# Kernel tuning notes

Hardware: AMD Instinct MI355X
Metric: run time of the kernel (lower is better)

The kernel has to match this reference:

```python
import jax, jax.numpy as jnp
import numpy as np

ALPHA = 30.0  # init kwarg alpha
K = 16        # init kwarg k


def setup_inputs() -> dict:
    key = jax.random.key(0)
    k1, k2 = jax.random.split(key)
    x = jax.random.normal(k1, (4096, 1024), dtype=jnp.float32)
    # L2-normalize embeddings (standard for metric-learning losses) so
    # pairwise distances lie in [0, 2] and exp(alpha*(1-d)) is well-scaled.
    x = x / jnp.linalg.norm(x, axis=1, keepdims=True)
    t = jax.random.randint(k2, (4096,), 0, 64)
    return {"inputs": x, "targets": t}


def _knn_softmax(inputs, targets):
    n = inputs.shape[0]
    # pairwise euclidean distances, clamp(1e-12).sqrt as in euclidean_dist
    sq = jnp.sum(inputs * inputs, axis=1)
    dist = sq[:, None] + sq[None, :] - 2.0 * (inputs @ inputs.T)
    dist = jnp.sqrt(jnp.clip(dist, 1e-12))  # [n, n]

    eye = jnp.eye(n, dtype=bool)
    same = targets[:, None] == targets[None, :]
    pos_mask = same & ~eye        # same label, off-diagonal
    neg_mask = ~same              # different label (diag excluded automatically)

    # threshold = (K+1)-th smallest off-diagonal distance per row
    # (equals sorted(concat(pos_pair, neg_pair))[K] in the original)
    BIG = jnp.float32(1e30)
    thr = jnp.sort(jnp.where(eye, BIG, dist), axis=1)[:, K]  # [n]

    below = dist < thr[:, None]
    logits = jnp.exp(ALPHA * (1.0 - dist))  # exp(alpha*(1 - d)) per pair

    pos_below = pos_mask & below
    neg_below = neg_mask & below
    pos_logit = jnp.sum(jnp.where(pos_below, logits, 0.0), axis=1)
    neg_logit = jnp.sum(jnp.where(neg_below, logits, 0.0), axis=1)

    # fallback: if no positive neighbor below threshold, use the first
    # positive pair (masked_select returns row order -> smallest index)
    first_pos = jnp.argmax(pos_mask, axis=1)
    fb = jnp.take_along_axis(logits, first_pos[:, None], axis=1)[:, 0]
    has_pos_below = jnp.any(pos_below, axis=1)
    pos_logit = jnp.where(has_pos_below, pos_logit, fb)

    loss_i = -jnp.log(pos_logit / (pos_logit + neg_logit))  # [n]

    # rows with no positive or no negative pair are skipped in the original
    valid = jnp.any(pos_mask, axis=1) & jnp.any(neg_mask, axis=1)
    n_valid = jnp.sum(valid.astype(jnp.float32))
    loss = jnp.sum(jnp.where(valid, loss_i, 0.0)) / n_valid
    accuracy = jnp.sum((valid & (loss_i < 0.6)).astype(jnp.float32)) / n
    return loss, accuracy


def reference(inputs, targets):
    loss, accuracy = _knn_softmax(inputs, targets)
    return (loss, accuracy, 0.0, 0.0)
```

## Files before the change

### kernel.cpp

```cpp
#include <hip/hip_runtime.h>
#include <hip/hip_bf16.h>
#include <cfloat>
#include <climits>
#include <cstdint>

#define ALPHA 30.0f
#define KSEL 16
#define P0 1.368f
#define P0SQ (P0 * P0)
#define CAP 224
#define TCAP 1664
#define BIGV 1e30f
#define NMAX 4096

typedef __attribute__((ext_vector_type(8))) short bf16x8;
typedef __attribute__((ext_vector_type(4))) float f32x4;
typedef __attribute__((ext_vector_type(8))) int i32x8;
typedef __attribute__((ext_vector_type(4))) int i32x4;

#define LDS_PTR(p) ((__attribute__((address_space(3))) uint32_t*)(p))
#define GLB_PTR(p) ((const __attribute__((address_space(1))) uint32_t*)(p))

__device__ inline float bfval(ushort u) {
    return __builtin_bit_cast(float, (uint32_t)u << 16);
}

__device__ inline float blockReduceSumF(float v, float* s) {
    for (int off = 32; off; off >>= 1) v += __shfl_down(v, off);
    int tid = threadIdx.x, wid = tid >> 6;
    if ((tid & 63) == 0) s[wid] = v;
    __syncthreads();
    float r;
    if (tid == 0) { r = s[0] + s[1] + s[2] + s[3]; s[0] = r; }
    __syncthreads();
    r = s[0];
    __syncthreads();
    return r;
}

__device__ inline int blockReduceSumI(int v, int* s) {
    for (int off = 32; off; off >>= 1) v += __shfl_down(v, off);
    int tid = threadIdx.x, wid = tid >> 6;
    if ((tid & 63) == 0) s[wid] = v;
    __syncthreads();
    int r;
    if (tid == 0) { r = s[0] + s[1] + s[2] + s[3]; s[0] = r; }
    __syncthreads();
    r = s[0];
    __syncthreads();
    return r;
}

__device__ inline int blockReduceMaxI(int v, int* s) {
    for (int off = 32; off; off >>= 1) v = max(v, __shfl_down(v, off));
    int tid = threadIdx.x, wid = tid >> 6;
    if ((tid & 63) == 0) s[wid] = v;
    __syncthreads();
    int r;
    if (tid == 0) { r = max(max(s[0], s[1]), max(s[2], s[3])); s[0] = r; }
    __syncthreads();
    r = s[0];
    __syncthreads();
    return r;
}

__global__ __launch_bounds__(256) void prep_kernel(const float* __restrict__ X,
                                                   ushort* __restrict__ Xbf,
                                                   uint32_t* __restrict__ Xb8,
                                                   float* __restrict__ sq,
                                                   const int* __restrict__ targets,
                                                   int* __restrict__ f1,
                                                   int* __restrict__ f2,
                                                   int* __restrict__ lcnt,
                                                   int D, int N) {
    __shared__ float sw[4];
    __shared__ int s1[4], s2[4], sc[4];
    int tid = threadIdx.x;
    int wid = tid >> 6;

    if (blockIdx.x >= (unsigned)N) {
        int lbl = blockIdx.x - N;
        int a1 = INT_MAX, a2 = INT_MAX, c = 0;
        for (int j = tid; j < N; j += 256) {
            if (targets[j] == lbl) {
                ++c;
                if (j < a1) { a2 = a1; a1 = j; }
                else if (j < a2) a2 = j;
            }
        }
        for (int off = 32; off; off >>= 1) {
            int b1 = __shfl_down(a1, off), b2 = __shfl_down(a2, off), bc = __shfl_down(c, off);
            int m1 = min(a1, b1);
            int m2 = min(max(a1, b1), min(a2, b2));
            a1 = m1; a2 = m2; c += bc;
        }
        if ((tid & 63) == 0) { s1[wid] = a1; s2[wid] = a2; sc[wid] = c; }
        __syncthreads();
        if (tid == 0) {
            int r1 = s1[0], r2 = s2[0], rc = sc[0];
            for (int w = 1; w < 4; ++w) {
                int m1 = min(r1, s1[w]);
                int m2 = min(max(r1, s1[w]), min(r2, s2[w]));
                r1 = m1; r2 = m2; rc += sc[w];
            }
            f1[lbl] = r1; f2[lbl] = r2; lcnt[lbl] = rc;
        }
        return;
    }

    int row = blockIdx.x;
    const float4* xr = reinterpret_cast<const float4*>(X + (size_t)row * D);
    ushort4* xo = reinterpret_cast<ushort4*>(Xbf + (size_t)row * D);
    uint32_t* x8o = Xb8 + (size_t)row * (D / 4);
    float s = 0.f;
    for (int c = tid; c < D / 4; c += 256) {
        float4 v = xr[c];
        s += v.x * v.x + v.y * v.y + v.z * v.z + v.w * v.w;
        ushort4 o;
        uint32_t b;
        b = __builtin_bit_cast(uint32_t, v.x); o.x = (ushort)((b + 0x7FFF + ((b >> 16) & 1)) >> 16);
        b = __builtin_bit_cast(uint32_t, v.y); o.y = (ushort)((b + 0x7FFF + ((b >> 16) & 1)) >> 16);
        b = __builtin_bit_cast(uint32_t, v.z); o.z = (ushort)((b + 0x7FFF + ((b >> 16) & 1)) >> 16);
        b = __builtin_bit_cast(uint32_t, v.w); o.w = (ushort)((b + 0x7FFF + ((b >> 16) & 1)) >> 16);
        xo[c] = o;
        int pk = __builtin_amdgcn_cvt_pk_fp8_f32(v.x * 16.f, v.y * 16.f, 0, false);
        pk = __builtin_amdgcn_cvt_pk_fp8_f32(v.z * 16.f, v.w * 16.f, pk, true);
        x8o[c] = (uint32_t)pk;
    }
    for (int off = 32; off; off >>= 1) s += __shfl_down(s, off);
    if ((tid & 63) == 0) sw[wid] = s;
    __syncthreads();
    if (tid == 0) sq[row] = sw[0] + sw[1] + sw[2] + sw[3];
}

#define GBM 256
#define GBK 128
__global__ __launch_bounds__(512, 2) void distgemm_mfma(const uint8_t* __restrict__ Xb8,
                                                        const float* __restrict__ sq,
                                                        float2* __restrict__ tileList,
                                                        int* __restrict__ tileCnt,
                                                        int* __restrict__ needFB,
                                                        int N, int D) {
    __shared__ uint8_t As[2][GBM * GBK];
    __shared__ uint8_t Bs[2][GBM * GBK];
    __shared__ float2 tlist[TCAP];
    __shared__ int s_cnt;

    int wg = blockIdx.x;
    int wgid = (wg & 7) * 32 + (wg >> 3);
    int by = wgid >> 4, bx = wgid & 15;

    int tid = threadIdx.x;
    int lane = tid & 63;
    int wave = tid >> 6;
    int waveM = wave >> 2;
    int waveN = wave & 3;

    int rowBase = by * GBM;
    int colBase = bx * GBM;

    if (tid == 0) s_cnt = 0;

    f32x4 acc[8][4];
#pragma unroll
    for (int m = 0; m < 8; ++m)
#pragma unroll
        for (int n2 = 0; n2 < 4; ++n2) {
            f32x4 z = {0.f, 0.f, 0.f, 0.f};
            acc[m][n2] = z;
        }

    int srow = lane >> 3;
    int sgb = ((lane & 7) << 4) ^ (srow << 4);
    auto STAGE = [&](int buf, int k0) {
#pragma unroll
        for (int p = 0; p < 4; ++p) {
            int r = p * 64 + wave * 8 + srow;
            const uint8_t* gA = Xb8 + (size_t)(rowBase + r) * D + k0 + sgb;
            const uint8_t* gB = Xb8 + (size_t)(colBase + r) * D + k0 + sgb;
            uint8_t* dA = &As[buf][p * 8192 + wave * 1024];
            uint8_t* dB = &Bs[buf][p * 8192 + wave * 1024];
            __builtin_amdgcn_global_load_lds(GLB_PTR(gA), LDS_PTR(dA), 16, 0, 0);
            __builtin_amdgcn_global_load_lds(GLB_PTR(gB), LDS_PTR(dB), 16, 0, 0);
        }
    };

    int nt = D / GBK;
    STAGE(0, 0);
    STAGE(1, GBK);

    int l15 = lane & 15;
    int kq32 = (lane >> 4) * 32;
    int rswz = (l15 & 7) << 4;

    for (int t = 0; t < nt; ++t) {
        if (t < nt - 1) {
            asm volatile("s_waitcnt vmcnt(8)" ::: "memory");
        } else {
            asm volatile("s_waitcnt vmcnt(0)" ::: "memory");
        }
        __builtin_amdgcn_sched_barrier(0);
        asm volatile("s_barrier" ::: "memory");

        const uint8_t* aB = As[t & 1];
        const uint8_t* bB = Bs[t & 1];

        __builtin_amdgcn_s_setprio(1);
        i32x8 bF[4];
#pragma unroll
        for (int n2 = 0; n2 < 4; ++n2) {
            int brl = waveN * 64 + n2 * 16 + l15;
            const uint8_t* base = bB + brl * 128;
            i32x4 lo = *reinterpret_cast<const i32x4*>(base + ((kq32) ^ rswz));
            i32x4 hi = *reinterpret_cast<const i32x4*>(base + ((kq32 + 16) ^ rswz));
            i32x8 f = {lo[0], lo[1], lo[2], lo[3], hi[0], hi[1], hi[2], hi[3]};
            bF[n2] = f;
        }
#pragma unroll
        for (int m = 0; m < 8; ++m) {
            int arl = waveM * 128 + m * 16 + l15;
            const uint8_t* base = aB + arl * 128;
            i32x4 lo = *reinterpret_cast<const i32x4*>(base + ((kq32) ^ rswz));
            i32x4 hi = *reinterpret_cast<const i32x4*>(base + ((kq32 + 16) ^ rswz));
            i32x8 aF = {lo[0], lo[1], lo[2], lo[3], hi[0], hi[1], hi[2], hi[3]};
#pragma unroll
            for (int n2 = 0; n2 < 4; ++n2)
                acc[m][n2] = __builtin_amdgcn_mfma_scale_f32_16x16x128_f8f6f4(
                    aF, bF[n2], acc[m][n2], 0, 0, 0, 0x7F, 0, 0x7F);
        }
        __builtin_amdgcn_s_setprio(0);

        asm volatile("s_barrier" ::: "memory");
        if (t + 2 < nt) STAGE(t & 1, (t + 2) * GBK);
    }

    __syncthreads();

    int cr = (lane >> 4) * 4;
    int cc = lane & 15;
    unsigned long long lmask_lt = (1ull << lane) - 1ull;
#pragma unroll
    for (int m = 0; m < 8; ++m) {
#pragma unroll
        for (int n2 = 0; n2 < 4; ++n2) {
            int gcol = colBase + waveN * 64 + n2 * 16 + cc;
            float sqc = sq[gcol];
#pragma unroll
            for (int r = 0; r < 4; ++r) {
                int grow = rowBase + waveM * 128 + m * 16 + cr + r;
                float v = sq[grow] + sqc - acc[m][n2][r] * 0.0078125f;
                bool pred = (v < P0SQ) && (grow != gcol);
                unsigned long long mask = __ballot(pred);
                if (mask) {
                    int leader = __ffsll((long long)mask) - 1;
                    int tot = __popcll(mask);
                    int base = 0;
                    if (lane == leader) base = atomicAdd(&s_cnt, tot);
                    base = __shfl(base, leader);
                    if (pred) {
                        int idx = base + __popcll(mask & lmask_lt);
                        if (idx < TCAP) {
                            float d = sqrtf(fmaxf(v, 1e-12f));
                            uint32_t pk = ((uint32_t)grow << 12) | (uint32_t)gcol;
                            float2 e; e.x = d; e.y = __builtin_bit_cast(float, pk);
                            tlist[idx] = e;
                        }
                    }
                }
            }
        }
    }
    __syncthreads();

    int cnt = s_cnt;
    int wr = min(cnt, TCAP);
    for (int e = tid; e < wr; e += 512)
        tileList[(size_t)wgid * TCAP + e] = tlist[e];
    if (tid == 0) tileCnt[wgid] = cnt;
    if (cnt > TCAP && tid < GBM)
        needFB[rowBase + tid] = 1;
}

__global__ __launch_bounds__(256) void bin_kernel(const float2* __restrict__ tileList,
                                                  const int* __restrict__ tileCnt,
                                                  float2* __restrict__ cand,
                                                  int* __restrict__ cntArr) {
    int t = blockIdx.x;
    int cnt = min(tileCnt[t], TCAP);
    for (int e = threadIdx.x; e < cnt; e += 256) {
        float2 v = tileList[(size_t)t * TCAP + e];
        uint32_t pk = __builtin_bit_cast(uint32_t, v.y);
        int i = (int)(pk >> 12), j = (int)(pk & 4095u);
        int p = atomicAdd(&cntArr[i], 1);
        if (p < CAP) {
            float2 e1; e1.x = v.x; e1.y = __builtin_bit_cast(float, j);
            cand[(size_t)i * CAP + p] = e1;
        }
    }
}

__global__ __launch_bounds__(256) void rowfinal_kernel(const float2* __restrict__ cand,
                                                       const int* __restrict__ cntArr,
                                                       const int* __restrict__ targets,
                                                       const ushort* __restrict__ Xbf,
                                                       const float* __restrict__ sq,
                                                       const int* __restrict__ f1,
                                                       const int* __restrict__ f2,
                                                       const int* __restrict__ lcnt,
                                                       int* __restrict__ needFB,
                                                       float* __restrict__ rowLoss,
                                                       int N, int D) {
    __shared__ float dbuf[4][CAP];
    int tid = threadIdx.x, lane = tid & 63, w = tid >> 6;
    int row = blockIdx.x * 4 + w;
    int ti = targets[row];
    int lc = lcnt[ti];
    bool validRow = (lc >= 2) && (lc < N);
    int cnt = cntArr[row];
    bool fb = (cnt < KSEL + 1) || (cnt > CAP);
    int lim = fb ? 0 : cnt;

    float ed[4]; int ej[4];
#pragma unroll
    for (int s = 0; s < 4; ++s) {
        int idx = lane + s * 64;
        bool in = (!fb) && (idx < cnt);
        if (in) {
            float2 e = cand[(size_t)row * CAP + idx];
            ed[s] = e.x; ej[s] = __builtin_bit_cast(int, e.y);
            dbuf[w][idx] = e.x;
        } else { ed[s] = BIGV; ej[s] = -1; }
    }
    __syncthreads();

    int rlo[4] = {0, 0, 0, 0}, req[4] = {0, 0, 0, 0};
    for (int q = 0; q < lim; ++q) {
        float u = dbuf[w][q];
#pragma unroll
        for (int s = 0; s < 4; ++s) {
            rlo[s] += (u < ed[s]);
            req[s] += (u == ed[s]);
        }
    }
    float thrc = BIGV;
#pragma unroll
    for (int s = 0; s < 4; ++s)
        if (ej[s] >= 0 && rlo[s] <= KSEL && KSEL < rlo[s] + req[s]) thrc = fminf(thrc, ed[s]);
    for (int off = 32; off; off >>= 1) thrc = fminf(thrc, __shfl_down(thrc, off));
    float thr = __shfl(thrc, 0);

    float posS = 0.f, negS = 0.f;
    int apb = 0;
#pragma unroll
    for (int s = 0; s < 4; ++s) {
        if (ej[s] >= 0 && ed[s] < thr) {
            bool same = (targets[ej[s]] == ti);
            float e = expf(ALPHA * (1.0f - ed[s]));
            if (same) { posS += e; apb = 1; }
            else negS += e;
        }
    }
    for (int off = 32; off; off >>= 1) {
        posS += __shfl_down(posS, off);
        negS += __shfl_down(negS, off);
        apb = max(apb, __shfl_down(apb, off));
    }

    int fp = 0;
    float dot = 0.f;
    if (validRow) {
        fp = (row == f1[ti]) ? f2[ti] : f1[ti];
        const ushort* xr = Xbf + (size_t)row * D;
        const ushort* xf = Xbf + (size_t)fp * D;
        for (int c = lane; c < D / 4; c += 64) {
            ushort4 a = *reinterpret_cast<const ushort4*>(xr + (size_t)c * 4);
            ushort4 b = *reinterpret_cast<const ushort4*>(xf + (size_t)c * 4);
            dot += bfval(a.x) * bfval(b.x) + bfval(a.y) * bfval(b.y)
                 + bfval(a.z) * bfval(b.z) + bfval(a.w) * bfval(b.w);
        }
    }
    for (int off = 32; off; off >>= 1) dot += __shfl_down(dot, off);

    if (lane == 0) {
        if (fb) {
            needFB[row] = 1;
        } else if (!validRow) {
            rowLoss[row] = BIGV;
        } else {
            float fbD = sqrtf(fmaxf(sq[row] + sq[fp] - 2.0f * dot, 1e-12f));
            float posLogit = apb ? posS : expf(ALPHA * (1.0f - fbD));
            rowLoss[row] = -logf(posLogit / (posLogit + negS));
        }
    }
}

__global__ __launch_bounds__(256) void fallback_kernel(const ushort* __restrict__ Xbf,
                                                       const float* __restrict__ sq,
                                                       const int* __restrict__ targets,
                                                       const int* __restrict__ needFB,
                                                       const int* __restrict__ f1,
                                                       const int* __restrict__ f2,
                                                       const int* __restrict__ lcnt,
                                                       float* __restrict__ rowLoss,
                                                       int N, int D) {
    int row = blockIdx.x;
    if (!needFB[row]) return;

    __shared__ float xrow[1024];
    __shared__ float rowD[NMAX];
    __shared__ float sF[4];
    __shared__ int sI[4];
    int tid = threadIdx.x;

    for (int k = tid; k < D; k += 256) xrow[k] = bfval(Xbf[(size_t)row * D + k]);
    __syncthreads();

    for (int j = tid; j < N; j += 256) {
        float dot = 0.f;
        const ushort* xj = Xbf + (size_t)j * D;
        for (int k = 0; k < D; ++k) dot += xrow[k] * bfval(xj[k]);
        rowD[j] = (j == row) ? BIGV
                             : sqrtf(fmaxf(sq[row] + sq[j] - 2.0f * dot, 1e-12f));
    }
    __syncthreads();

    uint32_t lo = 0, hi = 0x40800000u;
    while (lo < hi) {
        uint32_t mid = (lo + hi) >> 1;
        float mv = __builtin_bit_cast(float, mid);
        int c = 0;
        for (int j = tid; j < N; j += 256) c += (rowD[j] <= mv);
        c = blockReduceSumI(c, sI);
        if (c >= KSEL + 1) hi = mid; else lo = mid + 1;
    }
    float thr = __builtin_bit_cast(float, hi);

    int ti = targets[row];
    int lc = lcnt[ti];
    bool validRow = (lc >= 2) && (lc < N);

    float posS = 0.f, negS = 0.f;
    int apb = 0;
    for (int j = tid; j < N; j += 256) {
        if (j == row) continue;
        float d = rowD[j];
        bool same = (targets[j] == ti);
        if (d < thr) {
            float e = expf(ALPHA * (1.0f - d));
            if (same) { posS += e; apb = 1; }
            else negS += e;
        }
    }
    posS = blockReduceSumF(posS, sF);
    negS = blockReduceSumF(negS, sF);
    apb = blockReduceMaxI(apb, sI);

    if (tid == 0) {
        if (!validRow) { rowLoss[row] = BIGV; return; }
        int fp = (row == f1[ti]) ? f2[ti] : f1[ti];
        float posLogit = apb ? posS : expf(ALPHA * (1.0f - rowD[fp]));
        rowLoss[row] = -logf(posLogit / (posLogit + negS));
    }
}

__global__ __launch_bounds__(256) void reduce_kernel(const float* __restrict__ rowLoss,
                                                     float* __restrict__ out, int N) {
    __shared__ float sF[4];
    __shared__ int sI[4];
    int tid = threadIdx.x;
    float sumL = 0.f;
    int nValid = 0, nAcc = 0;
    for (int j = tid; j < N; j += 256) {
        float L = rowLoss[j];
        if (L != BIGV) {
            sumL += L;
            ++nValid;
            if (L < 0.6f) ++nAcc;
        }
    }
    sumL = blockReduceSumF(sumL, sF);
    nValid = blockReduceSumI(nValid, sI);
    nAcc = blockReduceSumI(nAcc, sI);
    if (tid == 0) {
        out[0] = (nValid > 0) ? sumL / (float)nValid : 0.f;
        out[1] = (float)nAcc / (float)N;
        out[2] = 0.f;
        out[3] = 0.f;
    }
}

extern "C" void kernel_launch(void* const* d_in, const int* in_sizes, int n_in,
                              void* d_out, int out_size, void* d_ws, size_t ws_size,
                              hipStream_t stream) {
    const float* X = (const float*)d_in[0];
    const int* targets = (const int*)d_in[1];
    float* out = (float*)d_out;

    int N = in_sizes[1];
    int D = in_sizes[0] / N;
    int tiles = N / GBM;
    int nTiles = tiles * tiles;

    float2* cand     = (float2*)d_ws;
    float2* tileList = cand + (size_t)N * CAP;
    float*  sq       = (float*)(tileList + (size_t)nTiles * TCAP);
    float*  rowLoss  = sq + N;
    int*    cntArr   = (int*)(rowLoss + N);
    int*    needFB   = cntArr + N;
    int*    tileCnt  = needFB + N;
    int*    f1       = tileCnt + nTiles;
    int*    f2       = f1 + 64;
    int*    lcnt     = f2 + 64;
    ushort* Xbf      = (ushort*)(lcnt + 64 + 64);
    uint32_t* Xb8    = (uint32_t*)(Xbf + (size_t)N * D);

    hipMemsetAsync(cntArr, 0, N * sizeof(int), stream);
    hipMemsetAsync(needFB, 0, N * sizeof(int), stream);

    prep_kernel<<<N + 64, 256, 0, stream>>>(X, Xbf, Xb8, sq, targets, f1, f2, lcnt, D, N);

    distgemm_mfma<<<nTiles, 512, 0, stream>>>((const uint8_t*)Xb8, sq, tileList,
                                              tileCnt, needFB, N, D);

    bin_kernel<<<nTiles, 256, 0, stream>>>(tileList, tileCnt, cand, cntArr);

    rowfinal_kernel<<<N / 4, 256, 0, stream>>>(cand, cntArr, targets, Xbf, sq,
                                               f1, f2, lcnt, needFB, rowLoss, N, D);

    fallback_kernel<<<N, 256, 0, stream>>>(Xbf, sq, targets, needFB,
                                           f1, f2, lcnt, rowLoss, N, D);

    reduce_kernel<<<1, 256, 0, stream>>>(rowLoss, out, N);
}
```

Baseline: 120.1 us.

## Interleave next-tile global-to-LDS prefetch with MFMA phases in GEMM main loop

Restructures the fp8 GEMM main loop from a depth-2 prefetch (staging tile t+2 after compute) into a one-tile-ahead scheme. The prefetch of tile t+1 is split into rounds issued between four MFMA sub-phases, each separated by barriers with priority raised around the MFMA bursts. The aim is to spread global loads across compute and interleave LDS reads with MFMA, in the style of ping-pong schedules. In exchange it waits on vmcnt(0) every iteration, leaving only one tile of lookahead, and adds several barriers per iteration.

```diff
diff --git a/kernel.cpp b/kernel.cpp
--- a/kernel.cpp
+++ b/kernel.cpp
@@ -172,66 +172,74 @@
 
     int srow = lane >> 3;
     int sgb = ((lane & 7) << 4) ^ (srow << 4);
-    auto STAGE = [&](int buf, int k0) {
-#pragma unroll
-        for (int p = 0; p < 4; ++p) {
-            int r = p * 64 + wave * 8 + srow;
-            const uint8_t* gA = Xb8 + (size_t)(rowBase + r) * D + k0 + sgb;
-            const uint8_t* gB = Xb8 + (size_t)(colBase + r) * D + k0 + sgb;
-            uint8_t* dA = &As[buf][p * 8192 + wave * 1024];
-            uint8_t* dB = &Bs[buf][p * 8192 + wave * 1024];
-            __builtin_amdgcn_global_load_lds(GLB_PTR(gA), LDS_PTR(dA), 16, 0, 0);
-            __builtin_amdgcn_global_load_lds(GLB_PTR(gB), LDS_PTR(dB), 16, 0, 0);
-        }
+    auto STAGE_ROUND = [&](int buf, int k0, int p) {
+        int r = p * 64 + wave * 8 + srow;
+        const uint8_t* gA = Xb8 + (size_t)(rowBase + r) * D + k0 + sgb;
+        const uint8_t* gB = Xb8 + (size_t)(colBase + r) * D + k0 + sgb;
+        uint8_t* dA = &As[buf][p * 8192 + wave * 1024];
+        uint8_t* dB = &Bs[buf][p * 8192 + wave * 1024];
+        __builtin_amdgcn_global_load_lds(GLB_PTR(gA), LDS_PTR(dA), 16, 0, 0);
+        __builtin_amdgcn_global_load_lds(GLB_PTR(gB), LDS_PTR(dB), 16, 0, 0);
     };
 
     int nt = D / GBK;
-    STAGE(0, 0);
-    STAGE(1, GBK);
+#pragma unroll
+    for (int p = 0; p < 4; ++p) STAGE_ROUND(0, 0, p);
 
     int l15 = lane & 15;
     int kq32 = (lane >> 4) * 32;
     int rswz = (l15 & 7) << 4;
 
     for (int t = 0; t < nt; ++t) {
-        if (t < nt - 1) {
-            asm volatile("s_waitcnt vmcnt(8)" ::: "memory");
-        } else {
-            asm volatile("s_waitcnt vmcnt(0)" ::: "memory");
-        }
+        asm volatile("s_waitcnt vmcnt(0)" ::: "memory");
         __builtin_amdgcn_sched_barrier(0);
-        asm volatile("s_barrier" ::: "memory");
+        __builtin_amdgcn_s_barrier();
 
         const uint8_t* aB = As[t & 1];
         const uint8_t* bB = Bs[t & 1];
-
-        __builtin_amdgcn_s_setprio(1);
+        int nslot = (t & 1) ^ 1;
+        bool pf = (t + 1 < nt);
+        int nk0 = (t + 1) * GBK;
+
         i32x8 bF[4];
 #pragma unroll
-        for (int n2 = 0; n2 < 4; ++n2) {
-            int brl = waveN * 64 + n2 * 16 + l15;
-            const uint8_t* base = bB + brl * 128;
-            i32x4 lo = *reinterpret_cast<const i32x4*>(base + ((kq32) ^ rswz));
-            i32x4 hi = *reinterpret_cast<const i32x4*>(base + ((kq32 + 16) ^ rswz));
-            i32x8 f = {lo[0], lo[1], lo[2], lo[3], hi[0], hi[1], hi[2], hi[3]};
-            bF[n2] = f;
-        }
-#pragma unroll
-        for (int m = 0; m < 8; ++m) {
-            int arl = waveM * 128 + m * 16 + l15;
-            const uint8_t* base = aB + arl * 128;
-            i32x4 lo = *reinterpret_cast<const i32x4*>(base + ((kq32) ^ rswz));
-            i32x4 hi = *reinterpret_cast<const i32x4*>(base + ((kq32 + 16) ^ rswz));
-            i32x8 aF = {lo[0], lo[1], lo[2], lo[3], hi[0], hi[1], hi[2], hi[3]};
-#pragma unroll
-            for (int n2 = 0; n2 < 4; ++n2)
-                acc[m][n2] = __builtin_amdgcn_mfma_scale_f32_16x16x128_f8f6f4(
-                    aF, bF[n2], acc[m][n2], 0, 0, 0, 0x7F, 0, 0x7F);
-        }
-        __builtin_amdgcn_s_setprio(0);
-
-        asm volatile("s_barrier" ::: "memory");
-        if (t + 2 < nt) STAGE(t & 1, (t + 2) * GBK);
+        for (int p = 0; p < 4; ++p) {
+            if (p == 0) {
+#pragma unroll
+                for (int n2 = 0; n2 < 4; ++n2) {
+                    int brl = waveN * 64 + n2 * 16 + l15;
+                    const uint8_t* base = bB + brl * 128;
+                    i32x4 lo = *reinterpret_cast<const i32x4*>(base + ((kq32) ^ rswz));
+                    i32x4 hi = *reinterpret_cast<const i32x4*>(base + ((kq32 + 16) ^ rswz));
+                    i32x8 f = {lo[0], lo[1], lo[2], lo[3], hi[0], hi[1], hi[2], hi[3]};
+                    bF[n2] = f;
+                }
+            }
+            i32x8 aF[2];
+#pragma unroll
+            for (int q = 0; q < 2; ++q) {
+                int arl = waveM * 128 + (2 * p + q) * 16 + l15;
+                const uint8_t* base = aB + arl * 128;
+                i32x4 lo = *reinterpret_cast<const i32x4*>(base + ((kq32) ^ rswz));
+                i32x4 hi = *reinterpret_cast<const i32x4*>(base + ((kq32 + 16) ^ rswz));
+                i32x8 f = {lo[0], lo[1], lo[2], lo[3], hi[0], hi[1], hi[2], hi[3]};
+                aF[q] = f;
+            }
+            if (pf && p < 2) {
+                STAGE_ROUND(nslot, nk0, 2 * p);
+                STAGE_ROUND(nslot, nk0, 2 * p + 1);
+            }
+            __builtin_amdgcn_s_barrier();
+            __builtin_amdgcn_s_setprio(1);
+#pragma unroll
+            for (int q = 0; q < 2; ++q)
+#pragma unroll
+                for (int n2 = 0; n2 < 4; ++n2)
+                    acc[2 * p + q][n2] = __builtin_amdgcn_mfma_scale_f32_16x16x128_f8f6f4(
+                        aF[q], bF[n2], acc[2 * p + q][n2], 0, 0, 0, 0x7F, 0, 0x7F);
+            __builtin_amdgcn_s_setprio(0);
+            __builtin_amdgcn_s_barrier();
+        }
     }
 
     __syncthreads();
```

Result: no change. 120.8 us (+0.6%).

## Exploit distance symmetry with upper-triangle tiles and fuse binning into GEMM

Applied to the files above, without the earlier changes.

The distance GEMM now launches a 2D grid of 128x128 tiles and returns early for lower-triangle blocks. Each candidate pair found in an off-diagonal tile is scattered into both row i's and row j's candidate lists, which roughly halves the GEMM work. The separate bin kernel and the global tileList round trip are removed: each tile writes its candidates straight from shared memory into the per-row lists. The price is that double-buffered async staging is replaced by a single-buffered load-then-sync loop, so memory latency is less hidden, and there are twice as many global atomics per pair.

```diff
diff --git a/kernel.cpp b/kernel.cpp
--- a/kernel.cpp
+++ b/kernel.cpp
@@ -9,11 +9,10 @@
 #define P0 1.368f
 #define P0SQ (P0 * P0)
 #define CAP 224
-#define TCAP 1664
+#define TCAP 512
 #define BIGV 1e30f
 #define NMAX 4096
 
-typedef __attribute__((ext_vector_type(8))) short bf16x8;
 typedef __attribute__((ext_vector_type(4))) float f32x4;
 typedef __attribute__((ext_vector_type(8))) int i32x8;
 typedef __attribute__((ext_vector_type(4))) int i32x4;
@@ -133,37 +132,37 @@
     if (tid == 0) sq[row] = sw[0] + sw[1] + sw[2] + sw[3];
 }
 
-#define GBM 256
+#define GBM 128
 #define GBK 128
-__global__ __launch_bounds__(512, 2) void distgemm_mfma(const uint8_t* __restrict__ Xb8,
-                                                        const float* __restrict__ sq,
-                                                        float2* __restrict__ tileList,
-                                                        int* __restrict__ tileCnt,
-                                                        int* __restrict__ needFB,
-                                                        int N, int D) {
-    __shared__ uint8_t As[2][GBM * GBK];
-    __shared__ uint8_t Bs[2][GBM * GBK];
+__global__ __launch_bounds__(256) void distgemm_mfma(const uint8_t* __restrict__ Xb8,
+                                                     const float* __restrict__ sq,
+                                                     float2* __restrict__ cand,
+                                                     int* __restrict__ cntArr,
+                                                     int* __restrict__ needFB,
+                                                     int N, int D) {
+    if (blockIdx.x < blockIdx.y) return;
+    __shared__ uint8_t As[GBM * GBK];
+    __shared__ uint8_t Bs[GBM * GBK];
     __shared__ float2 tlist[TCAP];
     __shared__ int s_cnt;
 
-    int wg = blockIdx.x;
-    int wgid = (wg & 7) * 32 + (wg >> 3);
-    int by = wgid >> 4, bx = wgid & 15;
+    int by = blockIdx.y, bx = blockIdx.x;
+    bool diag = (bx == by);
 
     int tid = threadIdx.x;
     int lane = tid & 63;
     int wave = tid >> 6;
-    int waveM = wave >> 2;
-    int waveN = wave & 3;
+    int waveR = wave >> 1;
+    int waveC = wave & 1;
 
     int rowBase = by * GBM;
     int colBase = bx * GBM;
 
     if (tid == 0) s_cnt = 0;
 
-    f32x4 acc[8][4];
-#pragma unroll
-    for (int m = 0; m < 8; ++m)
+    f32x4 acc[4][4];
+#pragma unroll
+    for (int m = 0; m < 4; ++m)
 #pragma unroll
         for (int n2 = 0; n2 < 4; ++n2) {
             f32x4 z = {0.f, 0.f, 0.f, 0.f};
@@ -172,54 +171,42 @@
 
     int srow = lane >> 3;
     int sgb = ((lane & 7) << 4) ^ (srow << 4);
-    auto STAGE = [&](int buf, int k0) {
+    auto STAGE = [&](int k0) {
 #pragma unroll
         for (int p = 0; p < 4; ++p) {
-            int r = p * 64 + wave * 8 + srow;
+            int c = wave * 4 + p;
+            int r = c * 8 + srow;
             const uint8_t* gA = Xb8 + (size_t)(rowBase + r) * D + k0 + sgb;
             const uint8_t* gB = Xb8 + (size_t)(colBase + r) * D + k0 + sgb;
-            uint8_t* dA = &As[buf][p * 8192 + wave * 1024];
-            uint8_t* dB = &Bs[buf][p * 8192 + wave * 1024];
-            __builtin_amdgcn_global_load_lds(GLB_PTR(gA), LDS_PTR(dA), 16, 0, 0);
-            __builtin_amdgcn_global_load_lds(GLB_PTR(gB), LDS_PTR(dB), 16, 0, 0);
+            __builtin_amdgcn_global_load_lds(GLB_PTR(gA), LDS_PTR(&As[c * 1024]), 16, 0, 0);
+            __builtin_amdgcn_global_load_lds(GLB_PTR(gB), LDS_PTR(&Bs[c * 1024]), 16, 0, 0);
         }
     };
-
-    int nt = D / GBK;
-    STAGE(0, 0);
-    STAGE(1, GBK);
 
     int l15 = lane & 15;
     int kq32 = (lane >> 4) * 32;
     int rswz = (l15 & 7) << 4;
+    int nt = D / GBK;
 
     for (int t = 0; t < nt; ++t) {
-        if (t < nt - 1) {
-            asm volatile("s_waitcnt vmcnt(8)" ::: "memory");
-        } else {
-            asm volatile("s_waitcnt vmcnt(0)" ::: "memory");
-        }
-        __builtin_amdgcn_sched_barrier(0);
-        asm volatile("s_barrier" ::: "memory");
-
-        const uint8_t* aB = As[t & 1];
-        const uint8_t* bB = Bs[t & 1];
-
-        __builtin_amdgcn_s_setprio(1);
+        STAGE(t * GBK);
+        __syncthreads();
+
         i32x8 bF[4];
 #pragma unroll
         for (int n2 = 0; n2 < 4; ++n2) {
-            int brl = waveN * 64 + n2 * 16 + l15;
-            const uint8_t* base = bB + brl * 128;
+            int brl = waveC * 64 + n2 * 16 + l15;
+            const uint8_t* base = Bs + brl * 128;
             i32x4 lo = *reinterpret_cast<const i32x4*>(base + ((kq32) ^ rswz));
             i32x4 hi = *reinterpret_cast<const i32x4*>(base + ((kq32 + 16) ^ rswz));
             i32x8 f = {lo[0], lo[1], lo[2], lo[3], hi[0], hi[1], hi[2], hi[3]};
             bF[n2] = f;
         }
-#pragma unroll
-        for (int m = 0; m < 8; ++m) {
-            int arl = waveM * 128 + m * 16 + l15;
-            const uint8_t* base = aB + arl * 128;
+        __builtin_amdgcn_s_setprio(1);
+#pragma unroll
+        for (int m = 0; m < 4; ++m) {
+            int arl = waveR * 64 + m * 16 + l15;
+            const uint8_t* base = As + arl * 128;
             i32x4 lo = *reinterpret_cast<const i32x4*>(base + ((kq32) ^ rswz));
             i32x4 hi = *reinterpret_cast<const i32x4*>(base + ((kq32 + 16) ^ rswz));
             i32x8 aF = {lo[0], lo[1], lo[2], lo[3], hi[0], hi[1], hi[2], hi[3]};
@@ -229,25 +216,21 @@
                     aF, bF[n2], acc[m][n2], 0, 0, 0, 0x7F, 0, 0x7F);
         }
         __builtin_amdgcn_s_setprio(0);
-
-        asm volatile("s_barrier" ::: "memory");
-        if (t + 2 < nt) STAGE(t & 1, (t + 2) * GBK);
-    }
-
-    __syncthreads();
+        __syncthreads();
+    }
 
     int cr = (lane >> 4) * 4;
     int cc = lane & 15;
     unsigned long long lmask_lt = (1ull << lane) - 1ull;
 #pragma unroll
-    for (int m = 0; m < 8; ++m) {
+    for (int m = 0; m < 4; ++m) {
 #pragma unroll
         for (int n2 = 0; n2 < 4; ++n2) {
-            int gcol = colBase + waveN * 64 + n2 * 16 + cc;
+            int gcol = colBase + waveC * 64 + n2 * 16 + cc;
             float sqc = sq[gcol];
 #pragma unroll
             for (int r = 0; r < 4; ++r) {
-                int grow = rowBase + waveM * 128 + m * 16 + cr + r;
+                int grow = rowBase + waveR * 64 + m * 16 + cr + r;
                 float v = sq[grow] + sqc - acc[m][n2][r] * 0.0078125f;
                 bool pred = (v < P0SQ) && (grow != gcol);
                 unsigned long long mask = __ballot(pred);
@@ -272,23 +255,9 @@
     }
     __syncthreads();
 
-    int cnt = s_cnt;
-    int wr = min(cnt, TCAP);
-    for (int e = tid; e < wr; e += 512)
-        tileList[(size_t)wgid * TCAP + e] = tlist[e];
-    if (tid == 0) tileCnt[wgid] = cnt;
-    if (cnt > TCAP && tid < GBM)
-        needFB[rowBase + tid] = 1;
-}
-
-__global__ __launch_bounds__(256) void bin_kernel(const float2* __restrict__ tileList,
-                                                  const int* __restrict__ tileCnt,
-                                                  float2* __restrict__ cand,
-                                                  int* __restrict__ cntArr) {
-    int t = blockIdx.x;
-    int cnt = min(tileCnt[t], TCAP);
-    for (int e = threadIdx.x; e < cnt; e += 256) {
-        float2 v = tileList[(size_t)t * TCAP + e];
+    int cnt = min(s_cnt, TCAP);
+    for (int e = tid; e < cnt; e += 256) {
+        float2 v = tlist[e];
         uint32_t pk = __builtin_bit_cast(uint32_t, v.y);
         int i = (int)(pk >> 12), j = (int)(pk & 4095u);
         int p = atomicAdd(&cntArr[i], 1);
@@ -296,6 +265,17 @@
             float2 e1; e1.x = v.x; e1.y = __builtin_bit_cast(float, j);
             cand[(size_t)i * CAP + p] = e1;
         }
+        if (!diag) {
+            int q = atomicAdd(&cntArr[j], 1);
+            if (q < CAP) {
+                float2 e2; e2.x = v.x; e2.y = __builtin_bit_cast(float, i);
+                cand[(size_t)j * CAP + q] = e2;
+            }
+        }
+    }
+    if (s_cnt > TCAP) {
+        if (tid < GBM) needFB[rowBase + tid] = 1;
+        else needFB[colBase + tid - GBM] = 1;
     }
 }
 
@@ -499,16 +479,13 @@
     int N = in_sizes[1];
     int D = in_sizes[0] / N;
     int tiles = N / GBM;
-    int nTiles = tiles * tiles;
 
     float2* cand     = (float2*)d_ws;
-    float2* tileList = cand + (size_t)N * CAP;
-    float*  sq       = (float*)(tileList + (size_t)nTiles * TCAP);
+    float*  sq       = (float*)(cand + (size_t)N * CAP);
     float*  rowLoss  = sq + N;
     int*    cntArr   = (int*)(rowLoss + N);
     int*    needFB   = cntArr + N;
-    int*    tileCnt  = needFB + N;
-    int*    f1       = tileCnt + nTiles;
+    int*    f1       = needFB + N;
     int*    f2       = f1 + 64;
     int*    lcnt     = f2 + 64;
     ushort* Xbf      = (ushort*)(lcnt + 64 + 64);
@@ -517,12 +494,12 @@
     hipMemsetAsync(cntArr, 0, N * sizeof(int), stream);
     hipMemsetAsync(needFB, 0, N * sizeof(int), stream);
 
-    prep_kernel<<<N + 64, 256, 0, stream>>>(X, Xbf, Xb8, sq, targets, f1, f2, lcnt, D, N);
-
-    distgemm_mfma<<<nTiles, 512, 0, stream>>>((const uint8_t*)Xb8, sq, tileList,
-                                              tileCnt, needFB, N, D);
-
-    bin_kernel<<<nTiles, 256, 0, stream>>>(tileList, tileCnt, cand, cntArr);
+    prep_kernel<<<N + 64, 256, 0, stream>>>(X, Xbf, Xb8, sq, targets,
+                                            f1, f2, lcnt, D, N);
+
+    dim3 grid(tiles, tiles);
+    distgemm_mfma<<<grid, 256, 0, stream>>>((const uint8_t*)Xb8, sq, cand,
+                                            cntArr, needFB, N, D);
 
     rowfinal_kernel<<<N / 4, 256, 0, stream>>>(cand, cntArr, targets, Xbf, sq,
                                                f1, f2, lcnt, needFB, rowLoss, N, D);
```

Result: faster. 113.3 us (-5.6%).
